# Performance work log

Measured on AMD Instinct MI355X. Metric: run time of the kernel, lower is better.

## Reference

```python
import jax, jax.numpy as jnp
import numpy as np
from jax import lax

ALPHA = 0.99
D_MODEL = 2048


def setup_inputs() -> dict:
    key = jax.random.key(0)
    x = jax.random.normal(key, (4, 4096, D_MODEL), dtype=jnp.float32)
    return {"x": x}


def reference(x) -> jnp.ndarray:
    # EMA recurrence: ema_t = alpha * ema_{t-1} + (1 - alpha) * x_t, ema_{-1} = 0
    b, s, d = x.shape
    alpha = jnp.asarray(ALPHA, dtype=x.dtype)
    one_m = jnp.asarray(1.0 - ALPHA, dtype=x.dtype)

    def step(ema, xt):  # ema: [b, d], xt: [b, d]
        ema = alpha * ema + one_m * xt
        return ema, ema

    ema0 = jnp.zeros((b, d), dtype=x.dtype)
    _, ys = lax.scan(step, ema0, jnp.swapaxes(x, 0, 1))  # ys: [s, b, d]
    return jnp.swapaxes(ys, 0, 1)  # [b, s, d]
```

## Files before the change

kernel.cpp:

```cpp
#include <hip/hip_runtime.h>


namespace {

constexpr int B  = 4;
constexpr int S  = 4096;
constexpr int D  = 2048;
constexpr int D4 = D / 4;
constexpr int NCHUNK = 32;
constexpr int L  = S / NCHUNK;
constexpr int NCOL4 = B * D4;
constexpr int BLOCK = 256;

constexpr float kA  = 0.99f;
constexpr float kOm = (float)(1.0 - 0.99);

__global__ __launch_bounds__(BLOCK)
void cema_k1_finals(const float4* __restrict__ x, float4* __restrict__ ws) {
    const int c  = blockIdx.x * BLOCK + threadIdx.x;
    const int j  = blockIdx.y;
    const int b  = c >> 9;
    const int d4 = c & (D4 - 1);

    const size_t base = ((size_t)b * S + (size_t)j * L) * D4 + d4;
    const float4* p = x + base;

    float e0 = 0.f, e1 = 0.f, e2 = 0.f, e3 = 0.f;
#pragma unroll 8
    for (int t = 0; t < L; ++t) {
        float4 v = p[(size_t)t * D4];
        e0 = kA * e0 + kOm * v.x;
        e1 = kA * e1 + kOm * v.y;
        e2 = kA * e2 + kOm * v.z;
        e3 = kA * e3 + kOm * v.w;
    }
    ws[(size_t)c * NCHUNK + j] = make_float4(e0, e1, e2, e3);
}

__global__ __launch_bounds__(BLOCK)
void cema_k2_apply(const float4* __restrict__ x, const float4* __restrict__ ws,
                   float4* __restrict__ out) {
    const int c  = blockIdx.x * BLOCK + threadIdx.x;
    const int j  = blockIdx.y;
    const int b  = c >> 9;
    const int d4 = c & (D4 - 1);

    float aL;
    {
        double t = 0.99;
        for (int i = 0; i < 7; ++i) t *= t;
        aL = (float)t;
    }

    float E0 = 0.f, E1 = 0.f, E2 = 0.f, E3 = 0.f;
    const float4* wsc = ws + (size_t)c * NCHUNK;
    for (int i = 0; i < j; ++i) {
        float4 f = wsc[i];
        E0 = E0 * aL + f.x;
        E1 = E1 * aL + f.y;
        E2 = E2 * aL + f.z;
        E3 = E3 * aL + f.w;
    }

    const size_t base = ((size_t)b * S + (size_t)j * L) * D4 + d4;
    const float4* p = x + base;
    float4* q = out + base;

#pragma unroll 8
    for (int t = 0; t < L; ++t) {
        float4 v = p[(size_t)t * D4];
        E0 = kA * E0 + kOm * v.x;
        E1 = kA * E1 + kOm * v.y;
        E2 = kA * E2 + kOm * v.z;
        E3 = kA * E3 + kOm * v.w;
        q[(size_t)t * D4] = make_float4(E0, E1, E2, E3);
    }
}

}

extern "C" void kernel_launch(void* const* d_in, const int* in_sizes, int n_in,
                              void* d_out, int out_size, void* d_ws, size_t ws_size,
                              hipStream_t stream) {
    const float4* x  = (const float4*)d_in[0];
    float4* out      = (float4*)d_out;
    float4* ws       = (float4*)d_ws;

    dim3 grid(NCOL4 / BLOCK, NCHUNK);
    cema_k1_finals<<<grid, BLOCK, 0, stream>>>(x, ws);
    cema_k2_apply <<<grid, BLOCK, 0, stream>>>(x, ws, out);
}
```

Before: 253.4 us.

## Templatize chunk count, transpose chunk-final layout, use nontemporal output stores

Makes the number of sequence chunks a template parameter and picks 128, 64 or 32 chunks according to the available workspace, raising parallelism and shortening each thread's serial recurrence. Chunk finals are now stored chunk-major so the prefix combine reads them coalesced across threads, and the chunk decay factor becomes a compile-time constant. Output writes use nontemporal stores to avoid polluting cache. With more chunks, later chunks do a longer serial combine over prior finals, and the choice depends on workspace size.

Measured after the change: 253.2 us. No clear change (-0.1%).

```diff
diff --git a/kernel.cpp b/kernel.cpp
--- a/kernel.cpp
+++ b/kernel.cpp
@@ -7,16 +7,24 @@
 constexpr int S  = 4096;
 constexpr int D  = 2048;
 constexpr int D4 = D / 4;
-constexpr int NCHUNK = 32;
-constexpr int L  = S / NCHUNK;
 constexpr int NCOL4 = B * D4;
 constexpr int BLOCK = 256;
+
+typedef float v4f __attribute__((ext_vector_type(4)));
 
 constexpr float kA  = 0.99f;
 constexpr float kOm = (float)(1.0 - 0.99);
 
+constexpr double alpha_pow_pow2(int l) {
+    double t = 0.99;
+    while (l > 1) { t *= t; l >>= 1; }
+    return t;
+}
+
+template <int NCHUNK>
 __global__ __launch_bounds__(BLOCK)
 void cema_k1_finals(const float4* __restrict__ x, float4* __restrict__ ws) {
+    constexpr int L = S / NCHUNK;
     const int c  = blockIdx.x * BLOCK + threadIdx.x;
     const int j  = blockIdx.y;
     const int b  = c >> 9;
@@ -34,28 +42,25 @@
         e2 = kA * e2 + kOm * v.z;
         e3 = kA * e3 + kOm * v.w;
     }
-    ws[(size_t)c * NCHUNK + j] = make_float4(e0, e1, e2, e3);
+    ws[(size_t)j * NCOL4 + c] = make_float4(e0, e1, e2, e3);
 }
 
+template <int NCHUNK>
 __global__ __launch_bounds__(BLOCK)
 void cema_k2_apply(const float4* __restrict__ x, const float4* __restrict__ ws,
                    float4* __restrict__ out) {
+    constexpr int L = S / NCHUNK;
+    constexpr float aL = (float)alpha_pow_pow2(L);
+
     const int c  = blockIdx.x * BLOCK + threadIdx.x;
     const int j  = blockIdx.y;
     const int b  = c >> 9;
     const int d4 = c & (D4 - 1);
 
-    float aL;
-    {
-        double t = 0.99;
-        for (int i = 0; i < 7; ++i) t *= t;
-        aL = (float)t;
-    }
-
     float E0 = 0.f, E1 = 0.f, E2 = 0.f, E3 = 0.f;
-    const float4* wsc = ws + (size_t)c * NCHUNK;
+#pragma unroll 4
     for (int i = 0; i < j; ++i) {
-        float4 f = wsc[i];
+        float4 f = ws[(size_t)i * NCOL4 + c];
         E0 = E0 * aL + f.x;
         E1 = E1 * aL + f.y;
         E2 = E2 * aL + f.z;
@@ -64,7 +69,7 @@
 
     const size_t base = ((size_t)b * S + (size_t)j * L) * D4 + d4;
     const float4* p = x + base;
-    float4* q = out + base;
+    v4f* q = (v4f*)(out + base);
 
 #pragma unroll 8
     for (int t = 0; t < L; ++t) {
@@ -73,8 +78,16 @@
         E1 = kA * E1 + kOm * v.y;
         E2 = kA * E2 + kOm * v.z;
         E3 = kA * E3 + kOm * v.w;
-        q[(size_t)t * D4] = make_float4(E0, E1, E2, E3);
+        v4f o = {E0, E1, E2, E3};
+        __builtin_nontemporal_store(o, &q[(size_t)t * D4]);
     }
+}
+
+template <int NCHUNK>
+void launch(const float4* x, float4* ws, float4* out, hipStream_t stream) {
+    dim3 grid(NCOL4 / BLOCK, NCHUNK);
+    cema_k1_finals<NCHUNK><<<grid, BLOCK, 0, stream>>>(x, ws);
+    cema_k2_apply<NCHUNK><<<grid, BLOCK, 0, stream>>>(x, ws, out);
 }
 
 }
@@ -86,7 +99,8 @@
     float4* out      = (float4*)d_out;
     float4* ws       = (float4*)d_ws;
 
-    dim3 grid(NCOL4 / BLOCK, NCHUNK);
-    cema_k1_finals<<<grid, BLOCK, 0, stream>>>(x, ws);
-    cema_k2_apply <<<grid, BLOCK, 0, stream>>>(x, ws, out);
+    const size_t per_chunk = (size_t)NCOL4 * sizeof(float4);
+    if (ws_size >= 128 * per_chunk)      launch<128>(x, ws, out, stream);
+    else if (ws_size >= 64 * per_chunk)  launch<64>(x, ws, out, stream);
+    else                                 launch<32>(x, ws, out, stream);
 }
```
